# Optimization experiments

Measured on AMD Instinct MI355X. Metric: run time of the kernel, lower is better.

Reference implementation:

```python
import jax, jax.numpy as jnp
import numpy as np

BERT_DIM = 768
N_ROWS = 5
N_COLS = 12
LN_EPS = 1e-5


def setup_inputs() -> dict:
    key = jax.random.key(0)
    ks = jax.random.split(key, 12)
    B, S = 256, 512
    token_hidden = jax.random.normal(ks[0], (B, S, BERT_DIM), dtype=jnp.float32)
    attention_mask = jax.random.randint(ks[1], (B, S), 0, 2, dtype=jnp.int32)
    s = lambda fan_in: 1.0 / np.sqrt(fan_in)
    return {
        "token_hidden": token_hidden,
        "attention_mask": attention_mask,
        # token_attention: Linear(768,128) -> Tanh -> Linear(128,1)
        "att_w1": jax.random.normal(ks[2], (128, BERT_DIM), dtype=jnp.float32) * s(BERT_DIM),
        "att_b1": jnp.zeros((128,), dtype=jnp.float32),
        "att_w2": jax.random.normal(ks[3], (1, 128), dtype=jnp.float32) * s(128),
        "att_b2": jnp.zeros((1,), dtype=jnp.float32),
        # feature_projector: Linear(768,256) -> GELU -> Dropout(eval) -> Linear(256,5)
        "proj_w1": jax.random.normal(ks[4], (256, BERT_DIM), dtype=jnp.float32) * s(BERT_DIM),
        "proj_b1": jnp.zeros((256,), dtype=jnp.float32),
        "proj_w2": jax.random.normal(ks[5], (N_ROWS, 256), dtype=jnp.float32) * s(256),
        "proj_b2": jnp.zeros((N_ROWS,), dtype=jnp.float32),
        # LayerNorm([5, 12])
        "ln_gamma": jnp.ones((N_ROWS, N_COLS), dtype=jnp.float32),
        "ln_beta": jnp.zeros((N_ROWS, N_COLS), dtype=jnp.float32),
    }


def reference(token_hidden, attention_mask, att_w1, att_b1, att_w2, att_b2,
              proj_w1, proj_b1, proj_w2, proj_b2, ln_gamma, ln_beta):
    # token attention scores: [B, S]
    h = jnp.tanh(jnp.einsum("bsd,hd->bsh", token_hidden, att_w1) + att_b1)
    scores = (jnp.einsum("bsh,oh->bso", h, att_w2) + att_b2)[..., 0]
    scores = jnp.where(attention_mask == 0, jnp.finfo(scores.dtype).min, scores)
    weights = jax.nn.softmax(scores, axis=-1)
    # top-k token selection (indices sorted ascending to preserve order)
    k = min(N_COLS, token_hidden.shape[1])
    _, top_idx = jax.lax.top_k(weights, k)  # [B, k]
    top_idx = jnp.sort(top_idx, axis=-1)
    selected = jnp.take_along_axis(token_hidden, top_idx[:, :, None], axis=1)  # [B, k, D]
    # feature projector (dropout is eval no-op)
    f = jax.nn.gelu(jnp.einsum("bkd,hd->bkh", selected, proj_w1) + proj_b1, approximate=False)
    f = jnp.einsum("bkh,rh->bkr", f, proj_w2) + proj_b2  # [B, k, n_rows]
    features = jnp.transpose(f, (0, 2, 1))  # [B, n_rows, k]
    if features.shape[-1] < N_COLS:
        features = jnp.pad(features, ((0, 0), (0, 0), (0, N_COLS - features.shape[-1])))
    # LayerNorm over trailing [n_rows, n_cols]
    mean = jnp.mean(features, axis=(-2, -1), keepdims=True)
    var = jnp.var(features, axis=(-2, -1), keepdims=True)
    return ln_gamma * (features - mean) * jax.lax.rsqrt(var + LN_EPS) + ln_beta
```

## Files before the change

### kernel.cpp

```cpp
#include <hip/hip_runtime.h>
#include <math.h>

#define B_BATCH 256
#define S_LEN   512
#define D_DIM   768
#define H_ATT   128
#define TOPK    12
#define NCAND   16
#define H_PROJ  256
#define N_ROWS  5
#define N_COLS  12

typedef __bf16 bf16x8 __attribute__((ext_vector_type(8)));
typedef float  f32x4  __attribute__((ext_vector_type(4)));

#define GLOBAL_AS __attribute__((address_space(1)))
#define LDS_AS    __attribute__((address_space(3)))

#define WS_SCORES 0
#define WS_WHI    524288
#define WS_WLO    720896
#define WS_W1Q    917504
#define WS_W1P    1310720

__global__ __launch_bounds__(256) void prep_kernel(
    const float* __restrict__ w1,
    const float* __restrict__ pw1,
    __bf16* __restrict__ whi, __bf16* __restrict__ wlo,
    float* __restrict__ w1q, float* __restrict__ w1p)
{
    int id = blockIdx.x * 256 + threadIdx.x;
    if (id < 98304) {
        int j    = id & 7;
        int lane = (id >> 3) & 63;
        int rest = id >> 9;
        int kt   = rest % 24;
        int nt   = rest / 24;
        int n = nt * 16 + (lane & 15);
        int k = kt * 32 + (lane >> 4) * 8 + j;
        float f = w1[n * D_DIM + k];
        __bf16 h = (__bf16)f;
        whi[id] = h;
        wlo[id] = (__bf16)(f - (float)h);
    } else if (id < 196608) {
        int e2 = id - 98304;
        int i  = e2 & 3;
        int n  = (e2 >> 2) & 127;
        int k4 = e2 >> 9;
        w1q[e2] = w1[n * D_DIM + k4 * 4 + i];
    } else {
        int e  = id - 196608;
        int i  = e & 3;
        int j  = (e >> 2) & 255;
        int k4 = e >> 10;
        w1p[e] = pw1[j * D_DIM + k4 * 4 + i];
    }
}

__device__ inline void split8(float4 a, float4 b, bf16x8& hi, bf16x8& lo) {
    float v[8] = {a.x, a.y, a.z, a.w, b.x, b.y, b.z, b.w};
#pragma unroll
    for (int i = 0; i < 8; ++i) {
        __bf16 h = (__bf16)v[i];
        hi[i] = h;
        lo[i] = (__bf16)(v[i] - (float)h);
    }
}

__global__ __launch_bounds__(256, 4) void score_mfma(
    const float*  __restrict__ th,
    const __bf16* __restrict__ whi,
    const __bf16* __restrict__ wlo,
    const float*  __restrict__ b1,
    const float*  __restrict__ w2,
    float* __restrict__ scores)
{
    __shared__ __bf16 Bs[2][2][8 * 512];

    const int tid = threadIdx.x;
    const int wv  = tid >> 6;
    const int ln  = tid & 63;

    const size_t row0 = (size_t)blockIdx.x * 128 + wv * 32 + (ln & 15);
    const float* pa0 = th + row0 * D_DIM + (ln >> 4) * 8;
    const float* pa1 = pa0 + 16 * D_DIM;

    auto stage = [&](int kt, int buf) {
#pragma unroll
        for (int q = 0; q < 4; ++q) {
            int s  = wv + q * 4;
            int hl = s >> 3;
            int nt = s & 7;
            const __bf16* src = (hl ? wlo : whi) +
                                (((size_t)nt * 24 + kt) * 64 + ln) * 8;
            __bf16* dst = &Bs[buf][hl][nt * 512];
            __builtin_amdgcn_global_load_lds(
                (GLOBAL_AS const void*)src, (LDS_AS void*)dst, 16, 0, 0);
        }
    };

    f32x4 acc[2][8];
    const f32x4 z = {0.f, 0.f, 0.f, 0.f};
#pragma unroll
    for (int i = 0; i < 2; ++i)
#pragma unroll
        for (int j = 0; j < 8; ++j) acc[i][j] = z;

    float4 c00 = *(const float4*)(pa0);
    float4 c01 = *(const float4*)(pa0 + 4);
    float4 c10 = *(const float4*)(pa1);
    float4 c11 = *(const float4*)(pa1 + 4);
    stage(0, 0);
    __syncthreads();

    for (int kt = 0; kt < 24; ++kt) {
        const int buf = kt & 1;
        float4 n00, n01, n10, n11;
        if (kt < 23) {
            n00 = *(const float4*)(pa0 + (kt + 1) * 32);
            n01 = *(const float4*)(pa0 + (kt + 1) * 32 + 4);
            n10 = *(const float4*)(pa1 + (kt + 1) * 32);
            n11 = *(const float4*)(pa1 + (kt + 1) * 32 + 4);
            stage(kt + 1, buf ^ 1);
        }

        bf16x8 ah0, al0, ah1, al1;
        split8(c00, c01, ah0, al0);
        split8(c10, c11, ah1, al1);

#pragma unroll
        for (int nt = 0; nt < 8; ++nt) {
            bf16x8 bh = *(bf16x8*)(&Bs[buf][0][nt * 512 + ln * 8]);
            bf16x8 bl = *(bf16x8*)(&Bs[buf][1][nt * 512 + ln * 8]);
            acc[0][nt] = __builtin_amdgcn_mfma_f32_16x16x32_bf16(ah0, bh, acc[0][nt], 0, 0, 0);
            acc[0][nt] = __builtin_amdgcn_mfma_f32_16x16x32_bf16(al0, bh, acc[0][nt], 0, 0, 0);
            acc[0][nt] = __builtin_amdgcn_mfma_f32_16x16x32_bf16(ah0, bl, acc[0][nt], 0, 0, 0);
            acc[1][nt] = __builtin_amdgcn_mfma_f32_16x16x32_bf16(ah1, bh, acc[1][nt], 0, 0, 0);
            acc[1][nt] = __builtin_amdgcn_mfma_f32_16x16x32_bf16(al1, bh, acc[1][nt], 0, 0, 0);
            acc[1][nt] = __builtin_amdgcn_mfma_f32_16x16x32_bf16(ah1, bl, acc[1][nt], 0, 0, 0);
        }
        if (kt < 23) {
            c00 = n00; c01 = n01; c10 = n10; c11 = n11;
            __syncthreads();
        }
    }

    const int col = ln & 15;
    float b1v[8], w2v[8];
#pragma unroll
    for (int nt = 0; nt < 8; ++nt) {
        b1v[nt] = b1[nt * 16 + col];
        w2v[nt] = w2[nt * 16 + col];
    }
    const size_t rowbase = (size_t)blockIdx.x * 128 + wv * 32;
#pragma unroll
    for (int mf = 0; mf < 2; ++mf)
#pragma unroll
        for (int r = 0; r < 4; ++r) {
            float s = 0.f;
#pragma unroll
            for (int nt = 0; nt < 8; ++nt)
                s += tanhf(acc[mf][nt][r] + b1v[nt]) * w2v[nt];
            s += __shfl_xor(s, 1, 64);
            s += __shfl_xor(s, 2, 64);
            s += __shfl_xor(s, 4, 64);
            s += __shfl_xor(s, 8, 64);
            if (col == 0)
                scores[rowbase + mf * 16 + (ln >> 4) * 4 + r] = s;
        }
}

__global__ __launch_bounds__(256) void select_kernel(
    const float* __restrict__ th,
    const int*   __restrict__ mask,
    const float* __restrict__ ascores,
    const float* __restrict__ w1q,
    const float* __restrict__ ab1,
    const float* __restrict__ aw2,
    const float* __restrict__ w1p,
    const float* __restrict__ pb1,
    const float* __restrict__ pw2,
    const float* __restrict__ pb2,
    const float* __restrict__ gamma,
    const float* __restrict__ beta,
    float* __restrict__ out)
{
    const int b   = blockIdx.x;
    const int tid = threadIdx.x;
    const int wv  = tid >> 6;
    const int ln  = tid & 63;

    __shared__ float4 xc[NCAND][192];
    __shared__ unsigned long long wtop[64];
    __shared__ int   cand[NCAND];
    __shared__ float redW[4][8];
    __shared__ float exact_sc[NCAND];
    __shared__ int   sel_slot[TOPK];
    __shared__ float gbuf[TOPK][H_PROJ + 4];
    __shared__ float feat[N_ROWS * N_COLS];
    __shared__ float stats[2];

    const float NEG_MIN = -3.402823466e38f;

    {
        int i0 = wv * 128 + ln, i1 = i0 + 64;
        float v0 = ascores[(size_t)b * S_LEN + i0];
        if (mask[(size_t)b * S_LEN + i0] == 0) v0 = NEG_MIN;
        float v1 = ascores[(size_t)b * S_LEN + i1];
        if (mask[(size_t)b * S_LEN + i1] == 0) v1 = NEG_MIN;
        unsigned k0 = __float_as_uint(v0);
        k0 = ((int)k0 >= 0) ? (k0 | 0x80000000u) : ~k0;
        unsigned k1 = __float_as_uint(v1);
        k1 = ((int)k1 >= 0) ? (k1 | 0x80000000u) : ~k1;
        unsigned long long p0 = ((unsigned long long)k0 << 32) | (0xFFFFFFFFu - (unsigned)i0);
        unsigned long long p1 = ((unsigned long long)k1 << 32) | (0xFFFFFFFFu - (unsigned)i1);
        for (int it = 0; it < NCAND; ++it) {
            unsigned long long m = p0 > p1 ? p0 : p1;
#pragma unroll
            for (int s = 1; s <= 32; s <<= 1) {
                unsigned long long o = __shfl_xor(m, s, 64);
                if (o > m) m = o;
            }
            if (ln == 0) wtop[wv * 16 + it] = m;
            if (p0 == m) p0 = 0ull;
            else if (p1 == m) p1 = 0ull;
        }
    }
    __syncthreads();
    if (wv == 0) {
        unsigned long long q = wtop[ln];
        for (int it = 0; it < NCAND; ++it) {
            unsigned long long m = q;
#pragma unroll
            for (int s = 1; s <= 32; s <<= 1) {
                unsigned long long o = __shfl_xor(m, s, 64);
                if (o > m) m = o;
            }
            if (ln == 0) cand[it] = (int)(0xFFFFFFFFu - (unsigned)(m & 0xFFFFFFFFu));
            if (q == m) q = 0ull;
        }
    }
    __syncthreads();

#pragma unroll
    for (int i = 0; i < 12; ++i) {
        int f = tid + 256 * i;
        int c = f / 192, k4 = f % 192;
        xc[c][k4] = *(const float4*)(th + ((size_t)b * S_LEN + cand[c]) * D_DIM + k4 * 4);
    }
    __syncthreads();

    {
        const int n = tid & 127;
        const int h = tid >> 7;
        float accs[8];
#pragma unroll
        for (int ci = 0; ci < 8; ++ci) accs[ci] = 0.f;
        for (int k4 = 0; k4 < 192; ++k4) {
            float4 w = *(const float4*)(w1q + (size_t)(k4 * 128 + n) * 4);
#pragma unroll
            for (int ci = 0; ci < 8; ++ci) {
                float4 x = xc[2 * ci + h][k4];
                accs[ci] += w.x * x.x + w.y * x.y + w.z * x.z + w.w * x.w;
            }
        }
        float b1n = ab1[n], w2n = aw2[n];
#pragma unroll
        for (int ci = 0; ci < 8; ++ci) {
            float val = tanhf(accs[ci] + b1n) * w2n;
            val += __shfl_xor(val, 1, 64);
            val += __shfl_xor(val, 2, 64);
            val += __shfl_xor(val, 4, 64);
            val += __shfl_xor(val, 8, 64);
            val += __shfl_xor(val, 16, 64);
            val += __shfl_xor(val, 32, 64);
            if (ln == 0) redW[wv][ci] = val;
        }
    }
    __syncthreads();
    if (tid < NCAND) {
        int c = tid;
        float ex = (c & 1) ? (redW[2][c >> 1] + redW[3][c >> 1])
                           : (redW[0][c >> 1] + redW[1][c >> 1]);
        if (mask[(size_t)b * S_LEN + cand[c]] == 0) ex = -INFINITY;
        exact_sc[c] = ex;
    }
    __syncthreads();

    if (tid == 0) {
        unsigned picked = 0;
        int slots[TOPK];
        for (int it = 0; it < TOPK; ++it) {
            float best = -INFINITY; int bslot = -1; int bidx = 1 << 30;
            for (int c = 0; c < NCAND; ++c) {
                if (picked & (1u << c)) continue;
                float e = exact_sc[c]; int idx = cand[c];
                if (e > best || (e == best && idx < bidx)) { best = e; bslot = c; bidx = idx; }
            }
            picked |= 1u << bslot;
            slots[it] = bslot;
        }
        for (int i = 1; i < TOPK; ++i) {
            int s = slots[i], key = cand[s], j = i - 1;
            while (j >= 0 && cand[slots[j]] > key) { slots[j + 1] = slots[j]; --j; }
            slots[j + 1] = s;
        }
        for (int t = 0; t < TOPK; ++t) sel_slot[t] = slots[t];
    }
    __syncthreads();

    {
        const int j = tid;
        int slots[TOPK];
#pragma unroll
        for (int t = 0; t < TOPK; ++t) slots[t] = sel_slot[t];
        float accp[TOPK];
        float bj = pb1[j];
#pragma unroll
        for (int t = 0; t < TOPK; ++t) accp[t] = bj;
        for (int k4 = 0; k4 < 192; ++k4) {
            float4 w = *(const float4*)(w1p + ((size_t)k4 * 256 + j) * 4);
#pragma unroll
            for (int t = 0; t < TOPK; ++t) {
                float4 x = xc[slots[t]][k4];
                accp[t] += w.x * x.x + w.y * x.y + w.z * x.z + w.w * x.w;
            }
        }
#pragma unroll
        for (int t = 0; t < TOPK; ++t) {
            float hh = accp[t];
            gbuf[t][j] = 0.5f * hh * (1.0f + erff(hh * 0.70710678118654752f));
        }
    }
    __syncthreads();

    if (tid < TOPK * N_ROWS) {
        int t = tid / N_ROWS, r = tid % N_ROWS;
        float s = pb2[r];
        const float4* gp = (const float4*)&gbuf[t][0];
        const float4* wp = (const float4*)(pw2 + r * H_PROJ);
        for (int q = 0; q < H_PROJ / 4; ++q) {
            float4 g = gp[q], w = wp[q];
            s += g.x * w.x + g.y * w.y + g.z * w.z + g.w * w.w;
        }
        feat[r * N_COLS + t] = s;
    }
    __syncthreads();

    if (tid == 0) {
        float sum = 0.f;
        for (int i = 0; i < N_ROWS * N_COLS; ++i) sum += feat[i];
        float mean = sum / 60.f;
        float sq = 0.f;
        for (int i = 0; i < N_ROWS * N_COLS; ++i) { float d = feat[i] - mean; sq += d * d; }
        stats[0] = mean;
        stats[1] = sq / 60.f;
    }
    __syncthreads();
    if (tid < N_ROWS * N_COLS) {
        float x = feat[tid];
        out[(size_t)b * 60 + tid] =
            gamma[tid] * (x - stats[0]) * rsqrtf(stats[1] + 1e-5f) + beta[tid];
    }
}

extern "C" void kernel_launch(void* const* d_in, const int* in_sizes, int n_in,
                              void* d_out, int out_size, void* d_ws, size_t ws_size,
                              hipStream_t stream) {
    const float* th   = (const float*)d_in[0];
    const int*   mask = (const int*)  d_in[1];
    const float* aw1  = (const float*)d_in[2];
    const float* ab1  = (const float*)d_in[3];
    const float* aw2  = (const float*)d_in[4];
    const float* pw1  = (const float*)d_in[6];
    const float* pb1  = (const float*)d_in[7];
    const float* pw2  = (const float*)d_in[8];
    const float* pb2  = (const float*)d_in[9];
    const float* gam  = (const float*)d_in[10];
    const float* bet  = (const float*)d_in[11];
    float* out = (float*)d_out;

    char* ws = (char*)d_ws;
    float*  scores = (float*)(ws + WS_SCORES);
    __bf16* whi    = (__bf16*)(ws + WS_WHI);
    __bf16* wlo    = (__bf16*)(ws + WS_WLO);
    float*  w1q    = (float*)(ws + WS_W1Q);
    float*  w1p    = (float*)(ws + WS_W1P);

    hipLaunchKernelGGL(prep_kernel, dim3(1536), dim3(256), 0, stream,
                       aw1, pw1, whi, wlo, w1q, w1p);
    hipLaunchKernelGGL(score_mfma, dim3(1024), dim3(256), 0, stream,
                       th, whi, wlo, ab1, aw2, scores);
    hipLaunchKernelGGL(select_kernel, dim3(B_BATCH), dim3(256), 0, stream,
                       th, mask, scores, w1q, ab1, aw2,
                       w1p, pb1, pw2, pb2, gam, bet, out);
}
```

Baseline: 727.7 us.

## Stage activation tiles into swizzled LDS via async global_load_lds

The fp32 token_hidden A-tile is no longer loaded straight into registers. It is now copied into a double-buffered LDS array with async global_load_lds and an XOR swizzle, then each wave reads its fragments from LDS. This is meant to coalesce the row-strided global loads and overlap them with MFMA work. The launch-bounds occupancy hint drops from 4 to 2, trading occupancy for a larger LDS footprint and more register room.

```diff
diff --git a/kernel.cpp b/kernel.cpp
--- a/kernel.cpp
+++ b/kernel.cpp
@@ -67,7 +67,7 @@
     }
 }
 
-__global__ __launch_bounds__(256, 4) void score_mfma(
+__global__ __launch_bounds__(256, 2) void score_mfma(
     const float*  __restrict__ th,
     const __bf16* __restrict__ whi,
     const __bf16* __restrict__ wlo,
@@ -75,15 +75,14 @@
     const float*  __restrict__ w2,
     float* __restrict__ scores)
 {
-    __shared__ __bf16 Bs[2][2][8 * 512];
+    __shared__ float  As[2][4096];
+    __shared__ __bf16 Bs[2][2][4096];
 
     const int tid = threadIdx.x;
     const int wv  = tid >> 6;
     const int ln  = tid & 63;
 
-    const size_t row0 = (size_t)blockIdx.x * 128 + wv * 32 + (ln & 15);
-    const float* pa0 = th + row0 * D_DIM + (ln >> 4) * 8;
-    const float* pa1 = pa0 + 16 * D_DIM;
+    const size_t arow = (size_t)blockIdx.x * 128;
 
     auto stage = [&](int kt, int buf) {
 #pragma unroll
@@ -93,9 +92,19 @@
             int nt = s & 7;
             const __bf16* src = (hl ? wlo : whi) +
                                 (((size_t)nt * 24 + kt) * 64 + ln) * 8;
-            __bf16* dst = &Bs[buf][hl][nt * 512];
             __builtin_amdgcn_global_load_lds(
-                (GLOBAL_AS const void*)src, (LDS_AS void*)dst, 16, 0, 0);
+                (GLOBAL_AS const void*)src,
+                (LDS_AS void*)&Bs[buf][hl][nt * 512], 16, 0, 0);
+        }
+#pragma unroll
+        for (int q = 0; q < 4; ++q) {
+            int s  = wv * 4 + q;
+            int r  = 8 * s + (ln >> 3);
+            int k4 = (ln & 7) ^ (ln >> 3);
+            const float* src = th + (arow + r) * D_DIM + kt * 32 + k4 * 4;
+            __builtin_amdgcn_global_load_lds(
+                (GLOBAL_AS const void*)src,
+                (LDS_AS void*)&As[buf][s * 256], 16, 0, 0);
         }
     };
 
@@ -106,32 +115,29 @@
 #pragma unroll
         for (int j = 0; j < 8; ++j) acc[i][j] = z;
 
-    float4 c00 = *(const float4*)(pa0);
-    float4 c01 = *(const float4*)(pa0 + 4);
-    float4 c10 = *(const float4*)(pa1);
-    float4 c11 = *(const float4*)(pa1 + 4);
     stage(0, 0);
     __syncthreads();
+
+    const int rl0 = wv * 32 + (ln & 15);
+    const int rx  = ln & 7;
+    const int c2  = (ln >> 4) * 2;
 
     for (int kt = 0; kt < 24; ++kt) {
         const int buf = kt & 1;
-        float4 n00, n01, n10, n11;
-        if (kt < 23) {
-            n00 = *(const float4*)(pa0 + (kt + 1) * 32);
-            n01 = *(const float4*)(pa0 + (kt + 1) * 32 + 4);
-            n10 = *(const float4*)(pa1 + (kt + 1) * 32);
-            n11 = *(const float4*)(pa1 + (kt + 1) * 32 + 4);
-            stage(kt + 1, buf ^ 1);
-        }
-
+        if (kt < 23) stage(kt + 1, buf ^ 1);
+
+        float4 a0 = *(const float4*)&As[buf][rl0 * 32 + ((c2    ) ^ rx) * 4];
+        float4 a1 = *(const float4*)&As[buf][rl0 * 32 + ((c2 + 1) ^ rx) * 4];
+        float4 a2 = *(const float4*)&As[buf][(rl0 + 16) * 32 + ((c2    ) ^ rx) * 4];
+        float4 a3 = *(const float4*)&As[buf][(rl0 + 16) * 32 + ((c2 + 1) ^ rx) * 4];
         bf16x8 ah0, al0, ah1, al1;
-        split8(c00, c01, ah0, al0);
-        split8(c10, c11, ah1, al1);
+        split8(a0, a1, ah0, al0);
+        split8(a2, a3, ah1, al1);
 
 #pragma unroll
         for (int nt = 0; nt < 8; ++nt) {
-            bf16x8 bh = *(bf16x8*)(&Bs[buf][0][nt * 512 + ln * 8]);
-            bf16x8 bl = *(bf16x8*)(&Bs[buf][1][nt * 512 + ln * 8]);
+            bf16x8 bh = *(const bf16x8*)(&Bs[buf][0][nt * 512 + ln * 8]);
+            bf16x8 bl = *(const bf16x8*)(&Bs[buf][1][nt * 512 + ln * 8]);
             acc[0][nt] = __builtin_amdgcn_mfma_f32_16x16x32_bf16(ah0, bh, acc[0][nt], 0, 0, 0);
             acc[0][nt] = __builtin_amdgcn_mfma_f32_16x16x32_bf16(al0, bh, acc[0][nt], 0, 0, 0);
             acc[0][nt] = __builtin_amdgcn_mfma_f32_16x16x32_bf16(ah0, bl, acc[0][nt], 0, 0, 0);
@@ -139,10 +145,7 @@
             acc[1][nt] = __builtin_amdgcn_mfma_f32_16x16x32_bf16(al1, bh, acc[1][nt], 0, 0, 0);
             acc[1][nt] = __builtin_amdgcn_mfma_f32_16x16x32_bf16(ah1, bl, acc[1][nt], 0, 0, 0);
         }
-        if (kt < 23) {
-            c00 = n00; c01 = n01; c10 = n10; c11 = n11;
-            __syncthreads();
-        }
+        if (kt < 23) __syncthreads();
     }
 
     const int col = ln & 15;
@@ -152,7 +155,7 @@
         b1v[nt] = b1[nt * 16 + col];
         w2v[nt] = w2[nt * 16 + col];
     }
-    const size_t rowbase = (size_t)blockIdx.x * 128 + wv * 32;
+    const size_t rowbase = arow + wv * 32;
 #pragma unroll
     for (int mf = 0; mf < 2; ++mf)
 #pragma unroll
```

After: 737.0 us. Within noise of the previous version (+1.3%).
